# Kernel optimization log

Hardware: AMD Instinct MI355X
Metric: run time of the kernel (lower is better)

Reference implementation:

```python
import jax, jax.numpy as jnp
import numpy as np

PROPOSAL_COUNT = 100
IOU_THRESHOLD = 0.5
SCORE_THRESHOLD = 0.05
IGNORE_LABEL = 0
PERFORMANCE_COUNT = 4096

B, N, C = 4, 100000, 80


def setup_inputs() -> dict:
    key = jax.random.key(0)
    k1, k2, k3, k4 = jax.random.split(key, 4)
    logits = jax.random.uniform(k1, (B, N, C), dtype=jnp.float32)
    regress = jax.random.uniform(k2, (B, N, 4), dtype=jnp.float32)
    points = jax.random.uniform(k3, (N, 2), dtype=jnp.float32)
    centerness = jax.random.uniform(k4, (B, N, 1), dtype=jnp.float32)
    return {"logits": logits, "regress": regress, "points": points, "centerness": centerness}


def offset2bbox(points, regress):
    return jnp.concatenate([points - regress[..., :2], points + regress[..., 2:]], axis=-1)


def pairwise_iou(boxes):
    # boxes: [K, 4] -> iou [K, K]
    area = (boxes[:, 2] - boxes[:, 0]) * (boxes[:, 3] - boxes[:, 1])
    lt = jnp.maximum(boxes[:, None, :2], boxes[None, :, :2])
    rb = jnp.minimum(boxes[:, None, 2:], boxes[None, :, 2:])
    wh = jnp.clip(rb - lt, 0.0)
    inter = wh[..., 0] * wh[..., 1]
    union = area[:, None] + area[None, :] - inter
    return inter / jnp.maximum(union, 1e-9)


def nms_image(logit, box):
    # logit: [N, C] (centerness-fused scores), box: [N, 4] decoded+clipped boxes
    n, c = logit.shape
    score = logit.at[:, IGNORE_LABEL].set(0.0)            # drop background class
    score = jnp.where(score > SCORE_THRESHOLD, score, 0.0)
    top_s, top_i = jax.lax.top_k(score.reshape(-1), PERFORMANCE_COUNT)  # over N*C pairs
    anchor = top_i // c
    cls = top_i % c
    cboxes = box[anchor]                                   # [K, 4]
    iou = pairwise_iou(cboxes)                             # [K, K]
    suppress = (iou > IOU_THRESHOLD) & (cls[:, None] == cls[None, :])

    def body(i, state):
        valid, sel = state
        s = jnp.where(valid, top_s, -1.0)
        j = jnp.argmax(s)
        ok = s[j] > 0.0
        sel = sel.at[i].set(jnp.where(ok, j.astype(jnp.int32), -1))
        valid = valid & ~suppress[j]
        valid = valid.at[j].set(False)
        return valid, sel

    valid0 = top_s > 0.0
    sel0 = jnp.full((PROPOSAL_COUNT,), -1, jnp.int32)
    _, sel = jax.lax.fori_loop(0, PROPOSAL_COUNT, body, (valid0, sel0))
    ok = sel >= 0
    selc = jnp.maximum(sel, 0)
    out_logit = jnp.where(ok[:, None], logit[anchor[selc]], 0.0)  # [P, C]
    out_box = jnp.where(ok[:, None], cboxes[selc], 0.0)           # [P, 4]
    return out_logit, out_box


def reference(logits, regress, points, centerness):
    fused = jnp.sqrt(logits * centerness)                        # centerness fusion
    boxes = jnp.clip(offset2bbox(points[None, :, :], regress), 0.0, 1.0)
    out_logit, out_box = jax.vmap(nms_image)(fused, boxes)
    return out_logit, out_box
```

## Files before the change

kernel.cpp:

```cpp
#include <hip/hip_runtime.h>
#include <cstdint>
#include <cstddef>

#define BB 4
#define NN 100000
#define CC 80
#define NC (NN * CC)
#define KTOP 4096
#define PROP 100
#define HBINS 10248
#define BUCKET_BASE 0x3D000u
#define CAPB 16384
#define SPILLCAP 131072
#define T0BK 0x3F733u
#define SPILL_LO (T0BK - BUCKET_BASE)
#define SPILL_BINS (HBINS - SPILL_LO)
#define P1CAP 1024

#define HIST_BYTES (BB * HBINS * 4)
#define CTRL_OFF   HIST_BYTES
#define ZERO_BYTES (HIST_BYTES + 128)
#define CANDA_OFF  (HIST_BYTES + 128)
#define CANDB_OFF  (CANDA_OFF + BB * KTOP * 8)
#define SPILL_OFF  (CANDB_OFF + BB * CAPB * 8)
#define WS_NEEDED  ((size_t)SPILL_OFF + (size_t)BB * SPILLCAP * 8)

__device__ __forceinline__ void agg_push(bool pred, unsigned long long pk,
                                         unsigned* counter, unsigned long long* buf,
                                         unsigned cap, int lane) {
    unsigned long long m = __ballot(pred);
    if (m) {
        int leader = __ffsll(m) - 1;
        unsigned base = 0;
        if (lane == leader) base = atomicAdd(counter, (unsigned)__popcll(m));
        base = (unsigned)__shfl((int)base, leader);
        if (pred) {
            unsigned pos = base + (unsigned)__popcll(m & ((1ull << lane) - 1ull));
            if (pos < cap) buf[pos] = pk;
        }
    }
}

__global__ void k_pass1(const float* __restrict__ logits, const float* __restrict__ cent,
                        unsigned* __restrict__ ctrl, unsigned long long* __restrict__ spill) {
    int b = blockIdx.y;
    __shared__ unsigned long long lbuf[P1CAP];
    __shared__ unsigned lcnt, gbase, lflush;
    if (threadIdx.x == 0) lcnt = 0;
    __syncthreads();
    const float4* lg = (const float4*)(logits + (size_t)b * NC);
    const float* cb = cent + (size_t)b * NN;
    const int T4 = NC / 4;
    for (int i = blockIdx.x * blockDim.x + threadIdx.x; i < T4; i += gridDim.x * blockDim.x) {
        float4 v = lg[i];
        int n = i / 20;
        int c4 = (i - n * 20) * 4;
        float ce = cb[n];
        unsigned k0 = __float_as_uint(sqrtf(v.x * ce));
        unsigned k1 = __float_as_uint(sqrtf(v.y * ce));
        unsigned k2 = __float_as_uint(sqrtf(v.z * ce));
        unsigned k3 = __float_as_uint(sqrtf(v.w * ce));
        bool p0 = (c4 != 0) && ((k0 >> 12) >= T0BK);
        bool p1 = (k1 >> 12) >= T0BK;
        bool p2 = (k2 >> 12) >= T0BK;
        bool p3 = (k3 >> 12) >= T0BK;
        unsigned cnt = (unsigned)p0 + (unsigned)p1 + (unsigned)p2 + (unsigned)p3;
        if (cnt) {
            unsigned q = atomicAdd(&lcnt, cnt);
            unsigned f = (unsigned)i * 4u;
            if (p0) { if (q < P1CAP) lbuf[q] = ((unsigned long long)k0 << 32) | (unsigned)(~(f + 0)); q++; }
            if (p1) { if (q < P1CAP) lbuf[q] = ((unsigned long long)k1 << 32) | (unsigned)(~(f + 1)); q++; }
            if (p2) { if (q < P1CAP) lbuf[q] = ((unsigned long long)k2 << 32) | (unsigned)(~(f + 2)); q++; }
            if (p3) { if (q < P1CAP) lbuf[q] = ((unsigned long long)k3 << 32) | (unsigned)(~(f + 3)); }
        }
    }
    __syncthreads();
    if (threadIdx.x == 0) {
        unsigned n = lcnt;
        if (n > P1CAP) { atomicOr(&ctrl[6], 1u); n = P1CAP; }
        lflush = n;
        gbase = n ? atomicAdd(&ctrl[b * 8 + 4], n) : 0u;
    }
    __syncthreads();
    unsigned long long* sp = spill + (size_t)b * SPILLCAP;
    unsigned n = lflush, g0 = gbase;
    for (unsigned i = threadIdx.x; i < n; i += blockDim.x) {
        unsigned pos = g0 + i;
        if (pos < SPILLCAP) sp[pos] = lbuf[i];
    }
}

__global__ void k_slowflag(unsigned* __restrict__ ctrl) {
    if (threadIdx.x == 0 && blockIdx.x == 0) {
        unsigned f = ctrl[6] ? 1u : 0u;
        for (int b = 0; b < BB; b++) {
            unsigned ns = ctrl[b * 8 + 4];
            if (ns < KTOP || ns > SPILLCAP) f = 1;
        }
        ctrl[7] = f;
    }
}

__global__ void k_hist_spill(const unsigned* __restrict__ ctrl,
                             const unsigned long long* __restrict__ spill,
                             unsigned* __restrict__ hist) {
    if (ctrl[7]) return;
    int b = blockIdx.y;
    __shared__ unsigned lh[SPILL_BINS];
    for (int i = threadIdx.x; i < SPILL_BINS; i += blockDim.x) lh[i] = 0;
    __syncthreads();
    unsigned ns = ctrl[b * 8 + 4];
    if (ns > SPILLCAP) ns = SPILLCAP;
    const unsigned long long* sp = spill + (size_t)b * SPILLCAP;
    for (unsigned i = blockIdx.x * blockDim.x + threadIdx.x; i < ns; i += gridDim.x * blockDim.x) {
        unsigned bits = (unsigned)(sp[i] >> 32);
        atomicAdd(&lh[(bits >> 12) - T0BK], 1u);
    }
    __syncthreads();
    unsigned* gh = hist + (size_t)b * HBINS + SPILL_LO;
    for (int i = threadIdx.x; i < SPILL_BINS; i += blockDim.x) {
        unsigned c = lh[i];
        if (c) atomicAdd(&gh[i], c);
    }
}

__global__ void k_hist(const float* __restrict__ logits, const float* __restrict__ cent,
                       unsigned* __restrict__ hist, const unsigned* __restrict__ ctrl) {
    if (ctrl[7] == 0) return;
    int b = blockIdx.y;
    __shared__ unsigned lh[HBINS];
    for (int i = threadIdx.x; i < HBINS; i += blockDim.x) lh[i] = 0;
    __syncthreads();
    const float4* lg = (const float4*)(logits + (size_t)b * NC);
    const float* cb = cent + (size_t)b * NN;
    const int T4 = NC / 4;
    for (int i = blockIdx.x * blockDim.x + threadIdx.x; i < T4; i += gridDim.x * blockDim.x) {
        float4 v = lg[i];
        int n = i / 20;
        int c4 = (i - n * 20) * 4;
        float ce = cb[n];
        float s;
        s = sqrtf(v.x * ce);
        if (c4 != 0 && s > 0.05f) atomicAdd(&lh[(__float_as_uint(s) >> 12) - BUCKET_BASE], 1u);
        s = sqrtf(v.y * ce);
        if (s > 0.05f) atomicAdd(&lh[(__float_as_uint(s) >> 12) - BUCKET_BASE], 1u);
        s = sqrtf(v.z * ce);
        if (s > 0.05f) atomicAdd(&lh[(__float_as_uint(s) >> 12) - BUCKET_BASE], 1u);
        s = sqrtf(v.w * ce);
        if (s > 0.05f) atomicAdd(&lh[(__float_as_uint(s) >> 12) - BUCKET_BASE], 1u);
    }
    __syncthreads();
    unsigned* gh = hist + (size_t)b * HBINS;
    for (int i = threadIdx.x; i < HBINS; i += blockDim.x) {
        unsigned c = lh[i];
        if (c) atomicAdd(&gh[i], c);
    }
}

__global__ void k_select(const unsigned* __restrict__ hist, unsigned* __restrict__ ctrl) {
    int b = blockIdx.x;
    int t = threadIdx.x;
    const unsigned* h = hist + (size_t)b * HBINS;
    __shared__ unsigned ssum[256];
    const int CH = (HBINS + 255) / 256;
    unsigned acc0 = 0;
    for (int i = 0; i < CH; i++) {
        int idx = t * CH + i;
        if (idx < HBINS) acc0 += h[idx];
    }
    ssum[t] = acc0;
    __syncthreads();
    for (int off = 1; off < 256; off <<= 1) {
        unsigned v = (t + off < 256) ? ssum[t + off] : 0u;
        __syncthreads();
        ssum[t] += v;
        __syncthreads();
    }
    unsigned acc = (t < 255) ? ssum[t + 1] : 0u;
    for (int i = CH - 1; i >= 0; i--) {
        int idx = t * CH + i;
        if (idx >= HBINS) continue;
        unsigned cnt = h[idx];
        unsigned na = acc + cnt;
        if (na >= KTOP && acc < KTOP) {
            ctrl[b * 8 + 0] = (unsigned)idx;
            ctrl[b * 8 + 1] = acc;
        }
        acc = na;
    }
}

__global__ void k_compact_fast(unsigned* __restrict__ ctrl,
                               const unsigned long long* __restrict__ spill,
                               unsigned long long* __restrict__ candA,
                               unsigned long long* __restrict__ candB) {
    if (ctrl[7]) return;
    int b = blockIdx.y;
    unsigned B1 = ctrl[b * 8 + 0];
    unsigned ns = ctrl[b * 8 + 4];
    if (ns > SPILLCAP) ns = SPILLCAP;
    const unsigned long long* sp = spill + (size_t)b * SPILLCAP;
    unsigned long long* gA = candA + (size_t)b * KTOP;
    unsigned long long* gB = candB + (size_t)b * CAPB;
    int lane = threadIdx.x & 63;
    unsigned TT = gridDim.x * blockDim.x;
    unsigned iters = (ns + TT - 1) / TT;
    for (unsigned k2 = 0; k2 < iters; k2++) {
        unsigned i = k2 * TT + blockIdx.x * blockDim.x + threadIdx.x;
        bool active = (i < ns);
        unsigned long long pk = active ? sp[i] : 0ull;
        unsigned bk = active ? (((unsigned)(pk >> 32)) >> 12) - BUCKET_BASE : 0u;
        bool pA = active && (bk > B1);
        bool pB = active && (bk == B1);
        agg_push(pA, pk, &ctrl[b * 8 + 2], gA, KTOP, lane);
        agg_push(pB, pk, &ctrl[b * 8 + 3], gB, CAPB, lane);
    }
}

__global__ void k_compact(const float* __restrict__ logits, const float* __restrict__ cent,
                          unsigned* __restrict__ ctrl,
                          unsigned long long* __restrict__ candA,
                          unsigned long long* __restrict__ candB) {
    if (ctrl[7] == 0) return;
    int b = blockIdx.y;
    unsigned B1 = ctrl[b * 8 + 0];
    const float4* lg = (const float4*)(logits + (size_t)b * NC);
    const float* cb = cent + (size_t)b * NN;
    const int T4 = NC / 4;
    unsigned long long* gA = candA + (size_t)b * KTOP;
    unsigned long long* gB = candB + (size_t)b * CAPB;
    for (int i = blockIdx.x * blockDim.x + threadIdx.x; i < T4; i += gridDim.x * blockDim.x) {
        float4 v = lg[i];
        int n = i / 20;
        int c4 = (i - n * 20) * 4;
        float ce = cb[n];
        float sv[4] = {v.x, v.y, v.z, v.w};
#pragma unroll
        for (int k = 0; k < 4; k++) {
            float s = sqrtf(sv[k] * ce);
            int c = c4 + k;
            if (c != 0 && s > 0.05f) {
                unsigned key = __float_as_uint(s);
                unsigned bk = (key >> 12) - BUCKET_BASE;
                if (bk >= B1) {
                    unsigned flat = (unsigned)(i * 4 + k);
                    unsigned long long pk = ((unsigned long long)key << 32) | (unsigned)(~flat);
                    if (bk > B1) {
                        unsigned p = atomicAdd(&ctrl[b * 8 + 2], 1u);
                        if (p < KTOP) gA[p] = pk;
                    } else {
                        unsigned p = atomicAdd(&ctrl[b * 8 + 3], 1u);
                        if (p < CAPB) gB[p] = pk;
                    }
                }
            }
        }
    }
}

__global__ void k_boundary(unsigned* __restrict__ ctrl,
                           unsigned long long* __restrict__ candA,
                           const unsigned long long* __restrict__ candB) {
    int b = blockIdx.x;
    int t = threadIdx.x;
    unsigned nA = ctrl[b * 8 + 2];
    if (nA > KTOP) nA = KTOP;
    unsigned nB = ctrl[b * 8 + 3];
    if (nB > CAPB) nB = CAPB;
    int m = (int)KTOP - (int)nA;
    if (m < 0) m = 0;
    __shared__ unsigned long long sB[8192];
    const unsigned long long* gB = candB + (size_t)b * CAPB;
    unsigned long long* gA = candA + (size_t)b * KTOP;
    unsigned nBr = (nB + 255u) & ~255u;
    for (unsigned ii = 0; ii < nBr; ii += 256) {
        unsigned i = ii + (unsigned)t;
        bool act = (i < nB);
        unsigned long long ki = act ? gB[i] : 0ull;
        unsigned rank = 0;
        for (unsigned cb0 = 0; cb0 < nB; cb0 += 8192) {
            unsigned chunk = nB - cb0;
            if (chunk > 8192) chunk = 8192;
            __syncthreads();
            for (unsigned j = (unsigned)t; j < chunk; j += 256) sB[j] = gB[cb0 + j];
            __syncthreads();
            if (act) {
                for (unsigned j = 0; j < chunk; j++) rank += (sB[j] > ki) ? 1u : 0u;
            }
        }
        if (act && rank < (unsigned)m) gA[nA + rank] = ki;
    }
    unsigned take = ((unsigned)m < nB) ? (unsigned)m : nB;
    unsigned filled = nA + take;
    for (unsigned i = filled + (unsigned)t; i < KTOP; i += 256) gA[i] = 0ull;
}

__global__ void __launch_bounds__(256, 1) k_nms(const float* __restrict__ logits,
                                                const float* __restrict__ regress,
                                                const float* __restrict__ points,
                                                const float* __restrict__ cent,
                                                const unsigned long long* __restrict__ candA,
                                                float* __restrict__ out) {
    int b = blockIdx.x;
    int t = threadIdx.x;
    const unsigned long long* gA = candA + (size_t)b * KTOP;

    __shared__ unsigned long long sk[KTOP];
    __shared__ float4 sbox[KTOP];
    __shared__ float4 kbox[PROP];
    __shared__ unsigned kcls[PROP];
    __shared__ unsigned selAnc[PROP];
    __shared__ unsigned scnt;

    for (int i = t; i < KTOP; i += 256) sk[i] = gA[i];
    if (t < PROP) { selAnc[t] = 0xFFFFFFFFu; kcls[t] = 0xFFFFFFFFu; }
    if (t == 0) scnt = 0;
    __syncthreads();

    for (unsigned k = 2; k <= KTOP; k <<= 1) {
        for (unsigned j = k >> 1; j > 0; j >>= 1) {
            for (unsigned t2 = t; t2 < KTOP / 2; t2 += 256) {
                unsigned i = ((t2 & ~(j - 1)) << 1) | (t2 & (j - 1));
                unsigned p2 = i + j;
                bool dir = ((i & k) == 0);
                unsigned long long a = sk[i], c = sk[p2];
                if ((a < c) == dir) { sk[i] = c; sk[p2] = a; }
            }
            __syncthreads();
        }
    }

    for (int i = t; i < KTOP; i += 256) {
        unsigned long long kk = sk[i];
        float4 bx = {0.f, 0.f, 0.f, 0.f};
        if (kk) {
            unsigned flat = ~(unsigned)kk;
            unsigned a = flat / CC;
            float px = points[a * 2 + 0], py = points[a * 2 + 1];
            const float* rg = regress + ((size_t)b * NN + a) * 4;
            bx.x = fminf(fmaxf(px - rg[0], 0.f), 1.f);
            bx.y = fminf(fmaxf(py - rg[1], 0.f), 1.f);
            bx.z = fminf(fmaxf(px + rg[2], 0.f), 1.f);
            bx.w = fminf(fmaxf(py + rg[3], 0.f), 1.f);
        }
        sbox[i] = bx;
    }
    __syncthreads();

    if (t < 64) {
        int lane = t;
        int cnt = 0;
        for (int i = 0; i < KTOP && cnt < PROP; i++) {
            unsigned long long kk = sk[i];
            if (kk == 0) break;
            unsigned flat = ~(unsigned)kk;
            unsigned a = flat / CC;
            unsigned ccls = flat - a * CC;
            float4 cb4 = sbox[i];
            float ca = (cb4.z - cb4.x) * (cb4.w - cb4.y);
            bool sup = false;
            if (lane < cnt) {
                float4 kb = kbox[lane];
                if (kcls[lane] == ccls) {
                    float w = fmaxf(fminf(cb4.z, kb.z) - fmaxf(cb4.x, kb.x), 0.f);
                    float h = fmaxf(fminf(cb4.w, kb.w) - fmaxf(cb4.y, kb.y), 0.f);
                    float inter = w * h;
                    float ka = (kb.z - kb.x) * (kb.w - kb.y);
                    float iou = inter / fmaxf(ca + ka - inter, 1e-9f);
                    sup = iou > 0.5f;
                }
            }
            if (lane + 64 < cnt) {
                float4 kb = kbox[lane + 64];
                if (kcls[lane + 64] == ccls) {
                    float w = fmaxf(fminf(cb4.z, kb.z) - fmaxf(cb4.x, kb.x), 0.f);
                    float h = fmaxf(fminf(cb4.w, kb.w) - fmaxf(cb4.y, kb.y), 0.f);
                    float inter = w * h;
                    float ka = (kb.z - kb.x) * (kb.w - kb.y);
                    float iou = inter / fmaxf(ca + ka - inter, 1e-9f);
                    sup = sup || (iou > 0.5f);
                }
            }
            if (!__any(sup)) {
                if (lane == 0) {
                    kbox[cnt] = cb4;
                    kcls[cnt] = ccls;
                    selAnc[cnt] = a;
                }
                cnt++;
            }
        }
        if (lane == 0) scnt = (unsigned)cnt;
    }
    __syncthreads();

    unsigned nk = scnt;
    float* outL = out + (size_t)b * PROP * CC;
    const float* lgb = logits + (size_t)b * NC;
    const float* cb = cent + (size_t)b * NN;
    for (int s = t; s < PROP * CC; s += 256) {
        int p = s / CC;
        int c = s - p * CC;
        float v = 0.f;
        if ((unsigned)p < nk) {
            unsigned a = selAnc[p];
            v = sqrtf(lgb[(size_t)a * CC + c] * cb[a]);
        }
        outL[s] = v;
    }
    float* outB = out + (size_t)BB * PROP * CC + (size_t)b * PROP * 4;
    for (int s = t; s < PROP * 4; s += 256) {
        int p = s >> 2;
        float v = 0.f;
        if ((unsigned)p < nk) v = ((const float*)&kbox[p])[s & 3];
        outB[s] = v;
    }
}

extern "C" void kernel_launch(void* const* d_in, const int* in_sizes, int n_in,
                              void* d_out, int out_size, void* d_ws, size_t ws_size,
                              hipStream_t stream) {
    const float* logits  = (const float*)d_in[0];
    const float* regress = (const float*)d_in[1];
    const float* points  = (const float*)d_in[2];
    const float* cent    = (const float*)d_in[3];
    float* out = (float*)d_out;

    char* ws = (char*)d_ws;
    unsigned* hist = (unsigned*)ws;
    unsigned* ctrl = (unsigned*)(ws + CTRL_OFF);
    unsigned long long* candA = (unsigned long long*)(ws + CANDA_OFF);
    unsigned long long* candB = (unsigned long long*)(ws + CANDB_OFF);
    unsigned long long* spill = (unsigned long long*)(ws + SPILL_OFF);

    hipMemsetAsync(d_ws, 0, ZERO_BYTES, stream);
    if (ws_size >= WS_NEEDED) {
        k_pass1<<<dim3(512, BB), 256, 0, stream>>>(logits, cent, ctrl, spill);
        k_slowflag<<<1, 64, 0, stream>>>(ctrl);
        k_hist_spill<<<dim3(32, BB), 256, 0, stream>>>(ctrl, spill, hist);
        k_hist<<<dim3(256, BB), 256, 0, stream>>>(logits, cent, hist, ctrl);
        k_select<<<BB, 256, 0, stream>>>(hist, ctrl);
        k_compact_fast<<<dim3(32, BB), 256, 0, stream>>>(ctrl, spill, candA, candB);
        k_compact<<<dim3(256, BB), 256, 0, stream>>>(logits, cent, ctrl, candA, candB);
    } else {
        hipMemsetAsync(ws + CTRL_OFF + 28, 1, 1, stream);
        k_hist<<<dim3(256, BB), 256, 0, stream>>>(logits, cent, hist, ctrl);
        k_select<<<BB, 256, 0, stream>>>(hist, ctrl);
        k_compact<<<dim3(256, BB), 256, 0, stream>>>(logits, cent, ctrl, candA, candB);
    }
    k_boundary<<<BB, 256, 0, stream>>>(ctrl, candA, candB);
    k_nms<<<BB, 256, 0, stream>>>(logits, regress, points, cent, candA, out);
}
```

Measured before the change: 398.2 us.

## Sort only top-bucket subset of candidates before NMS, fall back to full

Instead of bitonic-sorting all 4096 candidates, the NMS kernel builds a shared histogram of score buckets, selects roughly the top 512 candidates, sorts only those, and runs greedy NMS on them. If fewer than 100 boxes survive and unselected candidates remain, it retries with all candidates. Kept boxes and classes now live in per-lane registers instead of shared memory. The retry path adds cost when suppression is heavy, and the change adds a larger shared footprint.

```diff
diff --git a/kernel.cpp b/kernel.cpp
--- a/kernel.cpp
+++ b/kernel.cpp
@@ -16,6 +16,7 @@
 #define SPILL_LO (T0BK - BUCKET_BASE)
 #define SPILL_BINS (HBINS - SPILL_LO)
 #define P1CAP 1024
+#define NSEL 512
 
 #define HIST_BYTES (BB * HBINS * 4)
 #define CTRL_OFF   HIST_BYTES
@@ -306,95 +307,137 @@
     const unsigned long long* gA = candA + (size_t)b * KTOP;
 
     __shared__ unsigned long long sk[KTOP];
+    __shared__ unsigned long long sel[KTOP];
     __shared__ float4 sbox[KTOP];
+    __shared__ unsigned hist2[SPILL_BINS];
+    __shared__ unsigned sc[8];
     __shared__ float4 kbox[PROP];
-    __shared__ unsigned kcls[PROP];
     __shared__ unsigned selAnc[PROP];
-    __shared__ unsigned scnt;
-
-    for (int i = t; i < KTOP; i += 256) sk[i] = gA[i];
-    if (t < PROP) { selAnc[t] = 0xFFFFFFFFu; kcls[t] = 0xFFFFFFFFu; }
-    if (t == 0) scnt = 0;
-    __syncthreads();
-
-    for (unsigned k = 2; k <= KTOP; k <<= 1) {
-        for (unsigned j = k >> 1; j > 0; j >>= 1) {
-            for (unsigned t2 = t; t2 < KTOP / 2; t2 += 256) {
-                unsigned i = ((t2 & ~(j - 1)) << 1) | (t2 & (j - 1));
-                unsigned p2 = i + j;
-                bool dir = ((i & k) == 0);
-                unsigned long long a = sk[i], c = sk[p2];
-                if ((a < c) == dir) { sk[i] = c; sk[p2] = a; }
-            }
-            __syncthreads();
-        }
-    }
-
+
+    for (int i = t; i < SPILL_BINS; i += 256) hist2[i] = 0;
+    if (t < 8) sc[t] = 0;
+    __syncthreads();
     for (int i = t; i < KTOP; i += 256) {
-        unsigned long long kk = sk[i];
-        float4 bx = {0.f, 0.f, 0.f, 0.f};
+        unsigned long long kk = gA[i];
+        sk[i] = kk;
         if (kk) {
-            unsigned flat = ~(unsigned)kk;
-            unsigned a = flat / CC;
-            float px = points[a * 2 + 0], py = points[a * 2 + 1];
-            const float* rg = regress + ((size_t)b * NN + a) * 4;
-            bx.x = fminf(fmaxf(px - rg[0], 0.f), 1.f);
-            bx.y = fminf(fmaxf(py - rg[1], 0.f), 1.f);
-            bx.z = fminf(fmaxf(px + rg[2], 0.f), 1.f);
-            bx.w = fminf(fmaxf(py + rg[3], 0.f), 1.f);
-        }
-        sbox[i] = bx;
-    }
-    __syncthreads();
-
-    if (t < 64) {
-        int lane = t;
-        int cnt = 0;
-        for (int i = 0; i < KTOP && cnt < PROP; i++) {
+            int bkt = (int)((unsigned)(kk >> 32) >> 12) - (int)T0BK;
+            bkt = bkt < 0 ? 0 : bkt;
+            atomicAdd(&hist2[bkt], 1u);
+            atomicAdd(&sc[0], 1u);
+        }
+    }
+    __syncthreads();
+
+    for (int round = 0; round < 2; round++) {
+        unsigned target = round == 0 ? NSEL : KTOP;
+        if (t == 0) {
+            unsigned total = sc[0];
+            unsigned tgt = target < total ? target : total;
+            int bq = SPILL_BINS;
+            if (tgt > 0) {
+                unsigned acc = 0;
+                for (int i = SPILL_BINS - 1; i >= 0; i--) {
+                    acc += hist2[i];
+                    if (acc >= tgt) { bq = i; break; }
+                }
+            }
+            sc[2] = (unsigned)bq;
+            sc[1] = 0;
+            sc[3] = 0;
+            sc[4] = 0;
+        }
+        __syncthreads();
+        int bq = (int)sc[2];
+        for (int i = t; i < KTOP; i += 256) {
             unsigned long long kk = sk[i];
-            if (kk == 0) break;
-            unsigned flat = ~(unsigned)kk;
-            unsigned a = flat / CC;
-            unsigned ccls = flat - a * CC;
-            float4 cb4 = sbox[i];
-            float ca = (cb4.z - cb4.x) * (cb4.w - cb4.y);
-            bool sup = false;
-            if (lane < cnt) {
-                float4 kb = kbox[lane];
-                if (kcls[lane] == ccls) {
-                    float w = fmaxf(fminf(cb4.z, kb.z) - fmaxf(cb4.x, kb.x), 0.f);
-                    float h = fmaxf(fminf(cb4.w, kb.w) - fmaxf(cb4.y, kb.y), 0.f);
+            if (kk) {
+                int bkt = (int)((unsigned)(kk >> 32) >> 12) - (int)T0BK;
+                bkt = bkt < 0 ? 0 : bkt;
+                if (bkt >= bq) {
+                    unsigned p = atomicAdd(&sc[1], 1u);
+                    sel[p] = kk;
+                }
+            }
+        }
+        __syncthreads();
+        unsigned S = sc[1];
+        unsigned P2 = 2;
+        while (P2 < S) P2 <<= 1;
+        for (unsigned i = S + t; i < P2; i += 256) sel[i] = 0ull;
+        __syncthreads();
+        for (unsigned k = 2; k <= P2; k <<= 1) {
+            for (unsigned j = k >> 1; j > 0; j >>= 1) {
+                for (unsigned t2 = t; t2 < P2 / 2; t2 += 256) {
+                    unsigned i = ((t2 & ~(j - 1)) << 1) | (t2 & (j - 1));
+                    unsigned p2i = i + j;
+                    bool dir = ((i & k) == 0);
+                    unsigned long long a = sel[i], c = sel[p2i];
+                    if ((a < c) == dir) { sel[i] = c; sel[p2i] = a; }
+                }
+                __syncthreads();
+            }
+        }
+        for (unsigned i = t; i < S; i += 256) {
+            unsigned long long kk = sel[i];
+            float4 bx = {0.f, 0.f, 0.f, 0.f};
+            if (kk) {
+                unsigned flat = ~(unsigned)kk;
+                unsigned a = flat / CC;
+                float px = points[a * 2 + 0], py = points[a * 2 + 1];
+                const float* rg = regress + ((size_t)b * NN + a) * 4;
+                bx.x = fminf(fmaxf(px - rg[0], 0.f), 1.f);
+                bx.y = fminf(fmaxf(py - rg[1], 0.f), 1.f);
+                bx.z = fminf(fmaxf(px + rg[2], 0.f), 1.f);
+                bx.w = fminf(fmaxf(py + rg[3], 0.f), 1.f);
+            }
+            sbox[i] = bx;
+        }
+        __syncthreads();
+        if (t < 64) {
+            int lane = t;
+            float4 kb0 = {0, 0, 0, 0}, kb1 = {0, 0, 0, 0};
+            unsigned kc0 = 0xFFFFFFFFu, kc1 = 0xFFFFFFFFu;
+            int cnt = 0;
+            for (unsigned i = 0; i < S && cnt < PROP; i++) {
+                unsigned long long kk = sel[i];
+                if (!kk) break;
+                unsigned flat = ~(unsigned)kk;
+                unsigned a = flat / CC;
+                unsigned ccls = flat - a * CC;
+                float4 c4 = sbox[i];
+                float ca = (c4.z - c4.x) * (c4.w - c4.y);
+                bool sup = false;
+                if (lane < cnt && kc0 == ccls) {
+                    float w = fmaxf(fminf(c4.z, kb0.z) - fmaxf(c4.x, kb0.x), 0.f);
+                    float h = fmaxf(fminf(c4.w, kb0.w) - fmaxf(c4.y, kb0.y), 0.f);
                     float inter = w * h;
-                    float ka = (kb.z - kb.x) * (kb.w - kb.y);
-                    float iou = inter / fmaxf(ca + ka - inter, 1e-9f);
-                    sup = iou > 0.5f;
-                }
-            }
-            if (lane + 64 < cnt) {
-                float4 kb = kbox[lane + 64];
-                if (kcls[lane + 64] == ccls) {
-                    float w = fmaxf(fminf(cb4.z, kb.z) - fmaxf(cb4.x, kb.x), 0.f);
-                    float h = fmaxf(fminf(cb4.w, kb.w) - fmaxf(cb4.y, kb.y), 0.f);
+                    float ka = (kb0.z - kb0.x) * (kb0.w - kb0.y);
+                    sup = inter / fmaxf(ca + ka - inter, 1e-9f) > 0.5f;
+                }
+                if (lane + 64 < cnt && kc1 == ccls) {
+                    float w = fmaxf(fminf(c4.z, kb1.z) - fmaxf(c4.x, kb1.x), 0.f);
+                    float h = fmaxf(fminf(c4.w, kb1.w) - fmaxf(c4.y, kb1.y), 0.f);
                     float inter = w * h;
-                    float ka = (kb.z - kb.x) * (kb.w - kb.y);
-                    float iou = inter / fmaxf(ca + ka - inter, 1e-9f);
-                    sup = sup || (iou > 0.5f);
-                }
-            }
-            if (!__any(sup)) {
-                if (lane == 0) {
-                    kbox[cnt] = cb4;
-                    kcls[cnt] = ccls;
-                    selAnc[cnt] = a;
-                }
-                cnt++;
-            }
-        }
-        if (lane == 0) scnt = (unsigned)cnt;
-    }
-    __syncthreads();
-
-    unsigned nk = scnt;
+                    float ka = (kb1.z - kb1.x) * (kb1.w - kb1.y);
+                    sup = sup || (inter / fmaxf(ca + ka - inter, 1e-9f) > 0.5f);
+                }
+                if (!__any(sup)) {
+                    if (lane == cnt) { kb0 = c4; kc0 = ccls; }
+                    if (lane == cnt - 64) { kb1 = c4; kc1 = ccls; }
+                    if (lane == 0) { kbox[cnt] = c4; selAnc[cnt] = a; }
+                    cnt++;
+                }
+            }
+            if (lane == 0) sc[3] = (unsigned)cnt;
+        }
+        __syncthreads();
+        if (t == 0) sc[4] = (sc[3] < PROP && sc[1] < sc[0]) ? 1u : 0u;
+        __syncthreads();
+        if (!sc[4]) break;
+    }
+
+    unsigned nk = sc[3];
     float* outL = out + (size_t)b * PROP * CC;
     const float* lgb = logits + (size_t)b * NC;
     const float* cb = cent + (size_t)b * NN;
```

After: 329.0 us. 1.21x faster.
